# Kernel tuning notes

Measured on AMD Instinct MI355X. Metric: run time of the kernel, lower is better.

Reference implementation:

```python
import jax, jax.numpy as jnp
from jax import lax
import numpy as np

C = 256; NH = 8; NP = 4; FFN = 512; B = 2; H = 128; W = 128
HD = C // NH


def _ln(x, g, b):
    m = jnp.mean(x, -1, keepdims=True)
    v = jnp.var(x, -1, keepdims=True)
    return (x - m) * lax.rsqrt(v + 1e-5) * g + b


def _deform_attn(q, kv, off_w, off_b, attw_w, attw_b, vp_w, vp_b, op_w, op_b):
    # q, kv: (B, N, C) with N = H*W
    Bn, N, Cc = q.shape
    val = (kv @ vp_w + vp_b).reshape(Bn, N, NH, HD)
    off = (q @ off_w + off_b).reshape(Bn, N, NH, NP, 2)
    attw = jax.nn.softmax((q @ attw_w + attw_b).reshape(Bn, N, NH, NP), axis=-1)
    # identity-grid reference points (normalized, pixel centers)
    ry = (jnp.arange(H, dtype=q.dtype) + 0.5) / H
    rx = (jnp.arange(W, dtype=q.dtype) + 0.5) / W
    gy, gx = jnp.meshgrid(ry, rx, indexing='ij')
    ref = jnp.stack([gx.ravel(), gy.ravel()], -1)  # (N, 2) as (x, y)
    norm = jnp.array([W, H], dtype=q.dtype)
    loc = ref[None, :, None, None, :] + off / norm  # (B,N,NH,NP,2) in [0,1]
    # grid_sample align_corners=False, zeros padding
    x = loc[..., 0] * W - 0.5
    y = loc[..., 1] * H - 0.5
    x0 = jnp.floor(x); y0 = jnp.floor(y)
    lx = x - x0; ly = y - y0
    x0i = x0.astype(jnp.int32); y0i = y0.astype(jnp.int32)
    v_t = val.transpose(0, 2, 1, 3)  # (B, NH, N, HD)

    def gather(xi, yi, w):
        valid = (xi >= 0) & (xi < W) & (yi >= 0) & (yi < H)
        idx = jnp.clip(yi, 0, H - 1) * W + jnp.clip(xi, 0, W - 1)  # (B,N,NH,NP)
        idx_t = idx.transpose(0, 2, 1, 3).reshape(Bn, NH, N * NP)
        g = jnp.take_along_axis(v_t, idx_t[..., None], axis=2)
        g = g.reshape(Bn, NH, N, NP, HD)
        wm = (w * valid).transpose(0, 2, 1, 3)  # (B,NH,N,NP)
        return g * wm[..., None]

    samp = (gather(x0i, y0i, (1 - lx) * (1 - ly))
            + gather(x0i + 1, y0i, lx * (1 - ly))
            + gather(x0i, y0i + 1, (1 - lx) * ly)
            + gather(x0i + 1, y0i + 1, lx * ly))  # (B,NH,N,NP,HD)
    out = jnp.einsum('bhnpd,bnhp->bnhd', samp, attw).reshape(Bn, N, Cc)
    return out @ op_w + op_b


def _forward(cam_bev, sat_bev,
             c2s_off_w, c2s_off_b, c2s_attw_w, c2s_attw_b, c2s_vp_w, c2s_vp_b, c2s_op_w, c2s_op_b,
             s2c_off_w, s2c_off_b, s2c_attw_w, s2c_attw_b, s2c_vp_w, s2c_vp_b, s2c_op_w, s2c_op_b,
             ln1_g, ln1_b, ln2_g, ln2_b, lnf_g, lnf_b,
             ffn1_w, ffn1_b, ffn2_w, ffn2_b,
             g1_w, bn_g, bn_b, g2_w, g2_b):
    Bn, Cc, Hh, Ww = cam_bev.shape
    q_cam = cam_bev.reshape(Bn, Cc, Hh * Ww).transpose(0, 2, 1)
    q_sat = sat_bev.reshape(Bn, Cc, Hh * Ww).transpose(0, 2, 1)
    c2s = _deform_attn(q_cam, q_sat, c2s_off_w, c2s_off_b, c2s_attw_w, c2s_attw_b,
                       c2s_vp_w, c2s_vp_b, c2s_op_w, c2s_op_b)
    cam_att = _ln(q_cam + c2s, ln1_g, ln1_b)
    s2c = _deform_attn(q_sat, q_cam, s2c_off_w, s2c_off_b, s2c_attw_w, s2c_attw_b,
                       s2c_vp_w, s2c_vp_b, s2c_op_w, s2c_op_b)
    sat_att = _ln(q_sat + s2c, ln2_g, ln2_b)
    cam_map = cam_att.transpose(0, 2, 1).reshape(Bn, Cc, Hh, Ww)
    sat_map = sat_att.transpose(0, 2, 1).reshape(Bn, Cc, Hh, Ww)
    gi = jnp.concatenate([cam_map, sat_map], axis=1)
    h = lax.conv_general_dilated(gi, g1_w, (1, 1), 'SAME',
                                 dimension_numbers=('NCHW', 'OIHW', 'NCHW'))
    # BatchNorm2d in eval mode: running_mean=0, running_var=1
    h = jax.nn.relu(h * lax.rsqrt(jnp.float32(1.0 + 1e-5)) * bn_g[None, :, None, None]
                    + bn_b[None, :, None, None])
    g = jax.nn.sigmoid(jnp.einsum('bchw,oc->bohw', h, g2_w) + g2_b[None, :, None, None])
    fused = g * cam_map + (1 - g) * sat_map
    ff = fused.reshape(Bn, Cc, Hh * Ww).transpose(0, 2, 1)
    ff = ff + (jax.nn.relu(ff @ ffn1_w + ffn1_b) @ ffn2_w + ffn2_b)
    ff = _ln(ff, lnf_g, lnf_b)
    return ff.transpose(0, 2, 1).reshape(Bn, Cc, Hh, Ww) + cam_bev


def setup_inputs() -> dict:
    key = jax.random.key(0)
    ks = iter(jax.random.split(key, 40))

    def rn(shape, s=0.02):
        return jax.random.normal(next(ks), shape, jnp.float32) * s

    # directional offset-bias init (as in original init_weights)
    thetas = np.arange(NH) * (2.0 * np.pi / NH)
    grid = np.stack([np.cos(thetas), np.sin(thetas)], -1)
    grid = grid / np.abs(grid).max(-1, keepdims=True)
    grid = np.tile(grid[:, None, :], (1, NP, 1)) * np.arange(1, NP + 1)[None, :, None]
    off_bias = jnp.asarray(grid.reshape(-1), jnp.float32)

    def attn_params():
        return dict(off_w=rn((C, NH * NP * 2), 0.01), off_b=off_bias,
                    attw_w=rn((C, NH * NP), 0.02), attw_b=rn((NH * NP,), 0.02),
                    vp_w=rn((C, C), 0.05), vp_b=jnp.zeros((C,), jnp.float32),
                    op_w=rn((C, C), 0.05), op_b=jnp.zeros((C,), jnp.float32))

    p1 = attn_params(); p2 = attn_params()
    inp = {
        'cam_bev': jax.random.normal(next(ks), (B, C, H, W), jnp.float32),
        'sat_bev': jax.random.normal(next(ks), (B, C, H, W), jnp.float32),
    }
    for pre, p in (('c2s_', p1), ('s2c_', p2)):
        for k, v in p.items():
            inp[pre + k] = v
    inp.update(
        ln1_g=jnp.ones((C,), jnp.float32), ln1_b=jnp.zeros((C,), jnp.float32),
        ln2_g=jnp.ones((C,), jnp.float32), ln2_b=jnp.zeros((C,), jnp.float32),
        lnf_g=jnp.ones((C,), jnp.float32), lnf_b=jnp.zeros((C,), jnp.float32),
        ffn1_w=rn((C, FFN), 0.05), ffn1_b=jnp.zeros((FFN,), jnp.float32),
        ffn2_w=rn((FFN, C), 0.05), ffn2_b=jnp.zeros((C,), jnp.float32),
        g1_w=rn((C // 2, 2 * C, 3, 3), 0.02),
        bn_g=jnp.ones((C // 2,), jnp.float32), bn_b=jnp.zeros((C // 2,), jnp.float32),
        g2_w=rn((C, C // 2), 0.02), g2_b=jnp.zeros((C,), jnp.float32),
    )
    return inp


def reference(cam_bev, sat_bev,
              c2s_off_w, c2s_off_b, c2s_attw_w, c2s_attw_b, c2s_vp_w, c2s_vp_b, c2s_op_w, c2s_op_b,
              s2c_off_w, s2c_off_b, s2c_attw_w, s2c_attw_b, s2c_vp_w, s2c_vp_b, s2c_op_w, s2c_op_b,
              ln1_g, ln1_b, ln2_g, ln2_b, lnf_g, lnf_b,
              ffn1_w, ffn1_b, ffn2_w, ffn2_b,
              g1_w, bn_g, bn_b, g2_w, g2_b):
    return _forward(cam_bev, sat_bev,
                    c2s_off_w, c2s_off_b, c2s_attw_w, c2s_attw_b, c2s_vp_w, c2s_vp_b, c2s_op_w, c2s_op_b,
                    s2c_off_w, s2c_off_b, s2c_attw_w, s2c_attw_b, s2c_vp_w, s2c_vp_b, s2c_op_w, s2c_op_b,
                    ln1_g, ln1_b, ln2_g, ln2_b, lnf_g, lnf_b,
                    ffn1_w, ffn1_b, ffn2_w, ffn2_b,
                    g1_w, bn_g, bn_b, g2_w, g2_b)
```

## Files before the change

### kernel.cpp

```cpp
#include <hip/hip_runtime.h>
#include <hip/hip_bf16.h>
#include <cstddef>

#define BBn  2
#define CCn  256
#define HHn  128
#define WWn  128
#define NNn  (HHn*WWn)
#define MTOT (BBn*NNn)
#define PADW 130

typedef unsigned short u16;
typedef __attribute__((ext_vector_type(8))) short bf8v;
typedef __attribute__((ext_vector_type(8))) unsigned short u16x8;
typedef __attribute__((ext_vector_type(4))) float f4v;

typedef __attribute__((address_space(1))) const void gvoid_t;
typedef __attribute__((address_space(3))) void svoid_t;
#define ASYNC16(g, l) __builtin_amdgcn_global_load_lds((gvoid_t*)(g), (svoid_t*)(l), 16, 0, 0)

__device__ __forceinline__ u16 f2bf(float f) {
    __hip_bfloat16 h = __float2bfloat16(f);
    return *reinterpret_cast<u16*>(&h);
}
__device__ __forceinline__ float bf2f(u16 h) {
    return __uint_as_float(((unsigned)h) << 16);
}

struct ZOff {
    long a, w, bia, f1, f2, b1, r, p;
    int ch;
};

template<int BM, int BN, int WC, int EPI, int KK>
__global__ __launch_bounds__(256)
void mgemm(const u16* __restrict__ A, const u16* __restrict__ Wt,
           const float* __restrict__ bias, int ldw, int Nc,
           float* __restrict__ outf, float* __restrict__ outf2,
           u16* __restrict__ outb, const u16* __restrict__ img,
           const void* __restrict__ resid,
           const float* __restrict__ p0, const float* __restrict__ p1,
           int choff, ZOff zo)
{
    constexpr int WR = 4 / WC;
    constexpr int MROWS = BM / WR;
    constexpr int MI = MROWS / 16;
    constexpr int AT = BM / 64;
    constexpr int BT = BN / 64;

    __shared__ __align__(16) u16 As[BM * 32];
    __shared__ __align__(16) u16 Bs[BN * 32];
    __shared__ float red[4][64][2];

    const int z = blockIdx.z;
    if (z) {
        A += (long)z * zo.a; Wt += (long)z * zo.w;
        if (bias)  bias  += (long)z * zo.bia;
        if (outf)  outf  += (long)z * zo.f1;
        if (outf2) outf2 += (long)z * zo.f2;
        if (outb)  outb  += (long)z * zo.b1;
        if (p0)    p0    += (long)z * zo.p;
        if (p1)    p1    += (long)z * zo.p;
        choff += z * zo.ch;
    }

    const int tid  = threadIdx.x;
    const int lane = tid & 63;
    const int w    = tid >> 6;
    const int wr   = w / WC, wc = w % WC;
    const int by = blockIdx.y;
    const int m0 = by * BM;
    const int n0 = blockIdx.x * BN;
    const int lr = lane & 15, lq = lane >> 4;
    const int kb = lq * 8;

    const u16* gA[AT];
    #pragma unroll
    for (int t = 0; t < AT; ++t) {
        int c = t * 256 + tid; int row = c >> 2; int part = c & 3;
        gA[t] = A + (size_t)(m0 + row) * KK + part * 8;
    }
    const u16* gB[BT];
    #pragma unroll
    for (int t = 0; t < BT; ++t) {
        int c = t * 256 + tid; int row = c >> 2; int part = c & 3;
        gB[t] = Wt + (size_t)(n0 + row) * ldw + part * 8;
    }

    f4v acc[MI][4];
    if constexpr (EPI == 7 || EPI == 9) {
        const u16* r16 = (const u16*)resid + (EPI == 7 ? (long)z * zo.r : 0);
        #pragma unroll
        for (int j = 0; j < 4; ++j) {
            int n = wc * 64 + j * 16 + lr;
            float bj = bias[n];
            #pragma unroll
            for (int i = 0; i < MI; ++i)
                #pragma unroll
                for (int r = 0; r < 4; ++r) {
                    int m = m0 + i * 16 + lq * 4 + r;
                    acc[i][j][r] = bf2f(r16[(size_t)m * 256 + n]) + bj;
                }
        }
    } else {
        #pragma unroll
        for (int i = 0; i < MI; ++i)
            #pragma unroll
            for (int j = 0; j < 4; ++j)
                acc[i][j] = (f4v){0.f, 0.f, 0.f, 0.f};
    }

    for (int k0 = 0; k0 < KK; k0 += 32) {
        #pragma unroll
        for (int t = 0; t < AT; ++t)
            ASYNC16(gA[t] + k0, (u16*)As + (t * 256 + tid) * 8);
        #pragma unroll
        for (int t = 0; t < BT; ++t)
            ASYNC16(gB[t] + k0, (u16*)Bs + (t * 256 + tid) * 8);
        __syncthreads();

        bf8v af[MI], bv[4];
        #pragma unroll
        for (int i = 0; i < MI; ++i)
            af[i] = *(const bf8v*)&As[(wr * MROWS + i * 16 + lr) * 32 + kb];
        #pragma unroll
        for (int j = 0; j < 4; ++j)
            bv[j] = *(const bf8v*)&Bs[(wc * 64 + j * 16 + lr) * 32 + kb];
        #pragma unroll
        for (int i = 0; i < MI; ++i)
            #pragma unroll
            for (int j = 0; j < 4; ++j)
                acc[i][j] = __builtin_amdgcn_mfma_f32_16x16x32_bf16(af[i], bv[j], acc[i][j], 0, 0, 0);
        __syncthreads();
    }

    if constexpr (EPI == 7 || EPI == 9) {
        float g4[4], b4[4];
        #pragma unroll
        for (int j = 0; j < 4; ++j) {
            int n = wc * 64 + j * 16 + lr;
            g4[j] = p0[n]; b4[j] = p1[n];
        }
        #pragma unroll
        for (int i = 0; i < MI; ++i)
            #pragma unroll
            for (int r = 0; r < 4; ++r) {
                float p = 0.f, p2 = 0.f;
                #pragma unroll
                for (int j = 0; j < 4; ++j) { float v = acc[i][j][r]; p += v; p2 += v * v; }
                p += __shfl_xor(p, 1, 16);  p2 += __shfl_xor(p2, 1, 16);
                p += __shfl_xor(p, 2, 16);  p2 += __shfl_xor(p2, 2, 16);
                p += __shfl_xor(p, 4, 16);  p2 += __shfl_xor(p2, 4, 16);
                p += __shfl_xor(p, 8, 16);  p2 += __shfl_xor(p2, 8, 16);
                if (lr == 0) {
                    int row = i * 16 + lq * 4 + r;
                    red[w][row][0] = p; red[w][row][1] = p2;
                }
            }
        __syncthreads();
        #pragma unroll
        for (int i = 0; i < MI; ++i) {
            float mean4[4], rstd4[4];
            #pragma unroll
            for (int r = 0; r < 4; ++r) {
                int row = i * 16 + lq * 4 + r;
                float s  = red[0][row][0] + red[1][row][0] + red[2][row][0] + red[3][row][0];
                float s2 = red[0][row][1] + red[1][row][1] + red[2][row][1] + red[3][row][1];
                float mean = s * (1.f / 256.f);
                float var  = s2 * (1.f / 256.f) - mean * mean;
                mean4[r] = mean;
                rstd4[r] = rsqrtf(var + 1e-5f);
            }
            if constexpr (EPI == 7) {
                #pragma unroll
                for (int r = 0; r < 4; ++r) {
                    int m = m0 + i * 16 + lq * 4 + r;
                    int b = m >> 14, sp = m & (NNn - 1);
                    size_t pb = (((size_t)b * PADW + (sp >> 7) + 1) * PADW + (sp & 127) + 1) * 512 + choff;
                    #pragma unroll
                    for (int j = 0; j < 4; ++j) {
                        int n = wc * 64 + j * 16 + lr;
                        outb[pb + n] = f2bf((acc[i][j][r] - mean4[r]) * rstd4[r] * g4[j] + b4[j]);
                    }
                }
            } else {
                int mb = m0 + i * 16 + lq * 4;
                int b = mb >> 14, sp = mb & (NNn - 1);
                #pragma unroll
                for (int j = 0; j < 4; ++j) {
                    int n = wc * 64 + j * 16 + lr;
                    size_t oi = ((size_t)b * 256 + n) * NNn + sp;
                    float4 cv = *(const float4*)&outf2[oi];
                    float4 o;
                    o.x = (acc[i][j][0] - mean4[0]) * rstd4[0] * g4[j] + b4[j] + cv.x;
                    o.y = (acc[i][j][1] - mean4[1]) * rstd4[1] * g4[j] + b4[j] + cv.y;
                    o.z = (acc[i][j][2] - mean4[2]) * rstd4[2] * g4[j] + b4[j] + cv.z;
                    o.w = (acc[i][j][3] - mean4[3]) * rstd4[3] * g4[j] + b4[j] + cv.w;
                    *(float4*)&outf[oi] = o;
                }
            }
        }
        return;
    }

    float bj[4]; int ncol[4];
    #pragma unroll
    for (int j = 0; j < 4; ++j) {
        int n = n0 + wc * 64 + j * 16 + lr;
        ncol[j] = n;
        if constexpr (EPI == 0 || EPI == 4 || EPI == 5) bj[j] = bias[n];
    }
    #pragma unroll
    for (int i = 0; i < MI; ++i) {
        #pragma unroll
        for (int r = 0; r < 4; ++r) {
            int m = m0 + wr * MROWS + i * 16 + lq * 4 + r;
            size_t pb = 0;
            if constexpr (EPI == 4) {
                int b = m >> 14, sp = m & (NNn - 1);
                pb = (((size_t)b * PADW + (sp >> 7) + 1) * PADW + (sp & 127) + 1) * 512;
            }
            #pragma unroll
            for (int j = 0; j < 4; ++j) {
                int n = ncol[j];
                float v = acc[i][j][r];
                size_t oi = (size_t)m * Nc + n;
                if constexpr (EPI == 0) {
                    outb[oi] = f2bf(v + bj[j]);
                } else if constexpr (EPI == 2) {
                    if (n < 64)      outf [(size_t)m * 64 + n]        = v + p0[n];
                    else if (n < 96) outf2[(size_t)m * 32 + (n - 64)] = v + p1[n - 64];
                } else if constexpr (EPI == 4) {
                    float vv = v + bj[j];
                    float g = 1.f / (1.f + __expf(-vv));
                    float f = g * bf2f(img[pb + n]) + (1.f - g) * bf2f(img[pb + 256 + n]);
                    outb[oi] = f2bf(f);
                } else if constexpr (EPI == 5) {
                    outb[oi] = f2bf(fmaxf(v + bj[j], 0.f));
                }
            }
        }
    }
}

template<int TAPS>
__global__ __launch_bounds__(256)
void conv_k(const u16* __restrict__ img, const u16* __restrict__ Wt,
            float* __restrict__ outp)
{
    __shared__ __align__(16) u16 As[128 * 64];
    __shared__ __align__(16) u16 Bs[128 * 64];

    const int z = blockIdx.z;
    outp += (size_t)z * MTOT * 128;
    const int tid = threadIdx.x;
    const int lane = tid & 63;
    const int w = tid >> 6;
    const int wr = w >> 1, wc = w & 1;
    int by = blockIdx.y;
    by = ((by & 7) << 5) | (by >> 3);
    const int m0 = by * 128;
    const int lr = lane & 15, lq = lane >> 4;

    long cbA[4]; int pgA[4]; const u16* wB[4]; int ldsOff[4];
    #pragma unroll
    for (int t = 0; t < 4; ++t) {
        int c = t * 256 + tid;
        int row = c >> 3, part = c & 7;
        int pg = part ^ (row & 7);
        ldsOff[t] = c * 8;
        int m = m0 + row; int b = m >> 14; int sp = m & (NNn - 1);
        cbA[t] = ((long)b * PADW + (sp >> 7)) * PADW + (sp & 127);
        pgA[t] = pg;
        wB[t] = Wt + (size_t)row * 4608 + pg * 8;
    }

    f4v acc[4][4];
    #pragma unroll
    for (int i = 0; i < 4; ++i)
        #pragma unroll
        for (int j = 0; j < 4; ++j)
            acc[i][j] = (f4v){0.f, 0.f, 0.f, 0.f};

    const int tap0 = z * TAPS;
    #pragma unroll
    for (int tt = 0; tt < TAPS; ++tt) {
        int tap = tap0 + tt;
        int dy = tap / 3, dx = tap - dy * 3;
        const u16* bpA[4]; const u16* bpB[4];
        #pragma unroll
        for (int t = 0; t < 4; ++t) {
            bpA[t] = img + (size_t)(cbA[t] + dy * PADW + dx) * 512 + pgA[t] * 8;
            bpB[t] = wB[t] + tap * 512;
        }
        #pragma unroll 2
        for (int ci = 0; ci < 512; ci += 64) {
            #pragma unroll
            for (int t = 0; t < 4; ++t)
                ASYNC16(bpA[t] + ci, (u16*)As + ldsOff[t]);
            #pragma unroll
            for (int t = 0; t < 4; ++t)
                ASYNC16(bpB[t] + ci, (u16*)Bs + ldsOff[t]);
            __syncthreads();
            #pragma unroll
            for (int kk = 0; kk < 2; ++kk) {
                bf8v af[4], bv[4];
                #pragma unroll
                for (int i = 0; i < 4; ++i) {
                    int row = wr * 64 + i * 16 + lr;
                    af[i] = *(const bf8v*)&As[(row * 8 + ((kk * 4 + lq) ^ (row & 7))) * 8];
                }
                #pragma unroll
                for (int j = 0; j < 4; ++j) {
                    int row = wc * 64 + j * 16 + lr;
                    bv[j] = *(const bf8v*)&Bs[(row * 8 + ((kk * 4 + lq) ^ (row & 7))) * 8];
                }
                #pragma unroll
                for (int i = 0; i < 4; ++i)
                    #pragma unroll
                    for (int j = 0; j < 4; ++j)
                        acc[i][j] = __builtin_amdgcn_mfma_f32_16x16x32_bf16(af[i], bv[j], acc[i][j], 0, 0, 0);
            }
            __syncthreads();
        }
    }

    #pragma unroll
    for (int i = 0; i < 4; ++i)
        #pragma unroll
        for (int r = 0; r < 4; ++r) {
            int m = m0 + wr * 64 + i * 16 + lq * 4 + r;
            #pragma unroll
            for (int j = 0; j < 4; ++j) {
                int n = wc * 64 + j * 16 + lr;
                outp[(size_t)m * 128 + n] = acc[i][j][r];
            }
        }
}

__global__ __launch_bounds__(256)
void combine_k(const float* __restrict__ part, const float* __restrict__ bng,
               const float* __restrict__ bnb, u16* __restrict__ hb)
{
    const float bnscale = rsqrtf(1.0f + 1e-5f);
    int i = (blockIdx.x * 256 + threadIdx.x) * 4;
    int n = i & 127;
    float4 a = *(const float4*)&part[i];
    float4 b = *(const float4*)&part[(size_t)MTOT * 128 + i];
    float4 c = *(const float4*)&part[(size_t)MTOT * 256 + i];
    ushort4 o;
    o.x = f2bf(fmaxf((a.x + b.x + c.x) * bnscale * bng[n + 0] + bnb[n + 0], 0.f));
    o.y = f2bf(fmaxf((a.y + b.y + c.y) * bnscale * bng[n + 1] + bnb[n + 1], 0.f));
    o.z = f2bf(fmaxf((a.z + b.z + c.z) * bnscale * bng[n + 2] + bnb[n + 2], 0.f));
    o.w = f2bf(fmaxf((a.w + b.w + c.w) * bnscale * bng[n + 3] + bnb[n + 3], 0.f));
    *(ushort4*)&hb[i] = o;
}

__global__ __launch_bounds__(256)
void tcvt_k(const float* __restrict__ cam, const float* __restrict__ sat,
            u16* __restrict__ qcam, u16* __restrict__ qsat)
{
    __shared__ float t[64][65];
    int z = blockIdx.z;
    const float* src = (z < 2) ? cam : sat;
    u16* dst = (z < 2) ? qcam : qsat;
    int b = z & 1;
    int c0 = blockIdx.x * 64, sp0 = blockIdx.y * 64;
    #pragma unroll
    for (int it = 0; it < 16; ++it) {
        int idx = it * 256 + threadIdx.x;
        int cl = idx >> 6, sl = idx & 63;
        t[cl][sl] = src[((size_t)(b * CCn + c0 + cl)) * NNn + sp0 + sl];
    }
    __syncthreads();
    #pragma unroll
    for (int it = 0; it < 16; ++it) {
        int idx = it * 256 + threadIdx.x;
        int sl = idx >> 6, cl = idx & 63;
        dst[((size_t)(b * NNn + sp0 + sl)) * CCn + c0 + cl] = f2bf(t[cl][sl]);
    }
}

__global__ __launch_bounds__(256)
void sample_k(const u16* __restrict__ val, const float* __restrict__ off,
              const float* __restrict__ lg, u16* __restrict__ outp)
{
    __shared__ uint2 desc[32][17];

    int z = blockIdx.z;
    val  += (size_t)z * MTOT * CCn;
    off  += (size_t)z * MTOT * 64;
    lg   += (size_t)z * MTOT * 32;
    outp += (size_t)z * MTOT * CCn;

    const int tid = threadIdx.x;
    const int rh0 = blockIdx.x * 32;

    if (tid < 32) {
        int rhg = rh0 + tid;
        int h = rhg & 7, rn = rhg >> 3;
        int n = rn & (NNn - 1), b = rn >> 14;
        int yp = n >> 7, xp = n & 127;

        const float* ofp = off + (size_t)rn * 64 + h * 8;
        const float* lgp = lg  + (size_t)rn * 32 + h * 4;
        float4 of0 = *(const float4*)ofp;
        float4 of1 = *(const float4*)(ofp + 4);
        float4 lgv = *(const float4*)lgp;
        float ofx[4] = { of0.x, of0.z, of1.x, of1.z };
        float ofy[4] = { of0.y, of0.w, of1.y, of1.w };

        float mx = fmaxf(fmaxf(lgv.x, lgv.y), fmaxf(lgv.z, lgv.w));
        float e0 = __expf(lgv.x - mx), e1 = __expf(lgv.y - mx);
        float e2 = __expf(lgv.z - mx), e3 = __expf(lgv.w - mx);
        float inv = 1.f / (e0 + e1 + e2 + e3);
        float aw[4] = { e0 * inv, e1 * inv, e2 * inv, e3 * inv };

        unsigned hb = (unsigned)(b * NNn) * 256u + h * 32;
        #pragma unroll
        for (int p = 0; p < 4; ++p) {
            float xs = (float)xp + ofx[p];
            float ys = (float)yp + ofy[p];
            float x0f = floorf(xs), y0f = floorf(ys);
            float lx = xs - x0f, ly = ys - y0f;
            int x0 = (int)x0f, y0 = (int)y0f;
            #pragma unroll
            for (int c = 0; c < 4; ++c) {
                int xi = x0 + (c & 1), yi = y0 + (c >> 1);
                bool valid = (xi >= 0) & (xi < WWn) & (yi >= 0) & (yi < HHn);
                float wgt = valid
                    ? aw[p] * ((c & 1) ? lx : 1.f - lx) * ((c >> 1) ? ly : 1.f - ly)
                    : 0.f;
                int xc = min(max(xi, 0), WWn - 1);
                int yc = min(max(yi, 0), HHn - 1);
                unsigned addr = hb + (unsigned)(yc * WWn + xc) * 256u;
                desc[tid][p * 4 + c] = make_uint2(addr, __float_as_uint(wgt));
            }
        }
    }
    __syncthreads();

    const int rh = tid >> 3;
    const int q  = tid & 7;
    const int rhg = rh0 + rh;
    const int h = rhg & 7, rn = rhg >> 3;

    float a0 = 0.f, a1 = 0.f, a2 = 0.f, a3 = 0.f;
    #pragma unroll
    for (int k = 0; k < 16; ++k) {
        uint2 d = desc[rh][k];
        float wgt = __uint_as_float(d.y);
        ushort4 v = *(const ushort4*)(val + d.x + q * 4);
        a0 += wgt * bf2f(v.x);
        a1 += wgt * bf2f(v.y);
        a2 += wgt * bf2f(v.z);
        a3 += wgt * bf2f(v.w);
    }
    ushort4 o;
    o.x = f2bf(a0); o.y = f2bf(a1); o.z = f2bf(a2); o.w = f2bf(a3);
    *(ushort4*)(outp + (size_t)rn * CCn + h * 32 + q * 4) = o;
}

__global__ __launch_bounds__(256)
void repack_all(const float* __restrict__ vp1, const float* __restrict__ op1,
                const float* __restrict__ vp2, const float* __restrict__ op2,
                const float* __restrict__ f1w, const float* __restrict__ f2w,
                const float* __restrict__ of1, const float* __restrict__ aw1,
                const float* __restrict__ of2, const float* __restrict__ aw2,
                const float* __restrict__ g1,  const float* __restrict__ g2,
                const float* __restrict__ vpb1, const float* __restrict__ vpb2,
                const float* __restrict__ opb1, const float* __restrict__ opb2,
                const float* __restrict__ ofb1, const float* __restrict__ awb1,
                const float* __restrict__ ofb2, const float* __restrict__ awb2,
                const float* __restrict__ l1g, const float* __restrict__ l1b,
                const float* __restrict__ l2g, const float* __restrict__ l2b,
                u16* __restrict__ wb, float* __restrict__ bb)
{
    int i = blockIdx.x * 256 + threadIdx.x;
    if (i >= 1212416 + 2240) return;
    if (i >= 1212416) {
        int j = i - 1212416;
        float v;
        if      (j < 256)  v = vpb1[j];
        else if (j < 512)  v = vpb2[j - 256];
        else if (j < 768)  v = opb1[j - 512];
        else if (j < 1024) v = opb2[j - 768];
        else if (j < 1088) v = ofb1[j - 1024];
        else if (j < 1120) v = awb1[j - 1088];
        else if (j < 1184) v = ofb2[j - 1120];
        else if (j < 1216) v = awb2[j - 1184];
        else if (j < 1472) v = l1g[j - 1216];
        else if (j < 1728) v = l1b[j - 1472];
        else if (j < 1984) v = l2g[j - 1728];
        else               v = l2b[j - 1984];
        bb[j] = v;
        return;
    }
    float v;
    if (i < 262144) {
        const float* src[4] = { vp1, vp2, op1, op2 };
        int q = i >> 16, j = i & 65535;
        int n = j >> 8, k = j & 255;
        v = src[q][(size_t)k * 256 + n];
    } else if (i < 393216) {
        int j = i - 262144; int n = j >> 8, k = j & 255;
        v = f1w[(size_t)k * 512 + n];
    } else if (i < 524288) {
        int j = i - 393216; int n = j >> 9, k = j & 511;
        v = f2w[(size_t)k * 256 + n];
    } else if (i < 589824) {
        int jj = i - 524288; int hh = jj >> 15; int j = jj & 32767;
        int n = j >> 8, k = j & 255;
        const float* ofw = hh ? of2 : of1;
        const float* aww = hh ? aw2 : aw1;
        if (n < 64)      v = ofw[(size_t)k * 64 + n];
        else if (n < 96) v = aww[(size_t)k * 32 + (n - 64)];
        else             v = 0.f;
    } else if (i < 1179648) {
        int j = i - 589824; int co = j / 4608, k = j - co * 4608;
        int tap = k >> 9, ci = k & 511;
        v = g1[((size_t)co * 512 + ci) * 9 + tap];
    } else {
        int j = i - 1179648; int n = j >> 7, k = j & 127;
        v = g2[(size_t)n * 128 + k];
    }
    wb[i] = f2bf(v);
}

extern "C" void kernel_launch(void* const* d_in, const int* in_sizes, int n_in,
                              void* d_out, int out_size, void* d_ws, size_t ws_size,
                              hipStream_t stream)
{
    const float* cam_bev   = (const float*)d_in[0];
    const float* sat_bev   = (const float*)d_in[1];
    const float* c2s_off_w  = (const float*)d_in[2];
    const float* c2s_off_b  = (const float*)d_in[3];
    const float* c2s_attw_w = (const float*)d_in[4];
    const float* c2s_attw_b = (const float*)d_in[5];
    const float* c2s_vp_w   = (const float*)d_in[6];
    const float* c2s_vp_b   = (const float*)d_in[7];
    const float* c2s_op_w   = (const float*)d_in[8];
    const float* c2s_op_b   = (const float*)d_in[9];
    const float* s2c_off_w  = (const float*)d_in[10];
    const float* s2c_off_b  = (const float*)d_in[11];
    const float* s2c_attw_w = (const float*)d_in[12];
    const float* s2c_attw_b = (const float*)d_in[13];
    const float* s2c_vp_w   = (const float*)d_in[14];
    const float* s2c_vp_b   = (const float*)d_in[15];
    const float* s2c_op_w   = (const float*)d_in[16];
    const float* s2c_op_b   = (const float*)d_in[17];
    const float* ln1_g = (const float*)d_in[18];
    const float* ln1_b = (const float*)d_in[19];
    const float* ln2_g = (const float*)d_in[20];
    const float* ln2_b = (const float*)d_in[21];
    const float* lnf_g = (const float*)d_in[22];
    const float* lnf_b = (const float*)d_in[23];
    const float* ffn1_w = (const float*)d_in[24];
    const float* ffn1_b = (const float*)d_in[25];
    const float* ffn2_w = (const float*)d_in[26];
    const float* ffn2_b = (const float*)d_in[27];
    const float* g1_w  = (const float*)d_in[28];
    const float* bn_g  = (const float*)d_in[29];
    const float* bn_b  = (const float*)d_in[30];
    const float* g2_w  = (const float*)d_in[31];
    const float* g2_b  = (const float*)d_in[32];

    char* base = (char*)d_ws;
    size_t off = 0;
    auto alloc = [&](size_t bytes) -> void* {
        void* p = base + off;
        off += (bytes + 255) & ~(size_t)255;
        return p;
    };

    u16*   qcam   = (u16*)  alloc((size_t)MTOT * CCn * 2 * 2);
    u16*   qsat   = qcam + (size_t)MTOT * CCn;
    u16*   valb   = (u16*)  alloc((size_t)MTOT * CCn * 2 * 2);
    u16*   sampb  = (u16*)  alloc((size_t)MTOT * CCn * 2 * 2);
    float* offb   = (float*)alloc((size_t)MTOT * 64 * 4 * 2);
    float* attwb  = (float*)alloc((size_t)MTOT * 32 * 4 * 2);
    size_t padBytes = (size_t)BBn * PADW * PADW * 512 * 2;
    u16*   pad    = (u16*)  alloc(padBytes);
    u16*   hbuf   = (u16*)  alloc((size_t)MTOT * 128 * 2);
    u16*   wbase  = (u16*)  alloc((size_t)1212416 * 2);
    float* biasbf = (float*)alloc((size_t)2240 * 4);
    u16* wvp = wbase;
    u16* wop = wbase + 131072;
    u16* wf1 = wbase + 262144;
    u16* wf2 = wbase + 393216;
    u16* woa = wbase + 524288;
    u16* wcv = wbase + 589824;
    u16* wg2 = wbase + 1179648;
    u16*   fused_bf = valb;
    float* convpart = (float*)sampb;
    u16*   midb     = qcam;

    dim3 blk(256);
    ZOff zz{0, 0, 0, 0, 0, 0, 0, 0, 0};

    hipMemsetAsync(pad, 0, padBytes, stream);
    tcvt_k<<<dim3(4, 256, 4), blk, 0, stream>>>(cam_bev, sat_bev, qcam, qsat);
    repack_all<<<4746, blk, 0, stream>>>(c2s_vp_w, c2s_op_w, s2c_vp_w, s2c_op_w,
                                         ffn1_w, ffn2_w, c2s_off_w, c2s_attw_w,
                                         s2c_off_w, s2c_attw_w, g1_w, g2_w,
                                         c2s_vp_b, s2c_vp_b, c2s_op_b, s2c_op_b,
                                         c2s_off_b, c2s_attw_b, s2c_off_b, s2c_attw_b,
                                         ln1_g, ln1_b, ln2_g, ln2_b,
                                         wbase, biasbf);

    {
        ZOff zo{ -(long)MTOT * CCn, 65536, 256, 0, 0, (long)MTOT * CCn, 0, 0, 0 };
        mgemm<128, 128, 2, 0, 256><<<dim3(2, 256, 2), blk, 0, stream>>>(
            qsat, wvp, biasbf, 256, 256,
            nullptr, nullptr, valb, nullptr, nullptr, nullptr, nullptr, 0, zo);
    }
    {
        ZOff zo{ (long)MTOT * CCn, 32768, 0, (long)MTOT * 64, (long)MTOT * 32, 0, 0, 96, 0 };
        mgemm<128, 128, 2, 2, 256><<<dim3(1, 256, 2), blk, 0, stream>>>(
            qcam, woa, nullptr, 256, 128,
            offb, attwb, nullptr, nullptr, nullptr, biasbf + 1024, biasbf + 1088, 0, zo);
    }
    sample_k<<<dim3(8192, 1, 2), blk, 0, stream>>>(valb, offb, attwb, sampb);
    {
        ZOff zo{ (long)MTOT * CCn, 65536, 256, 0, 0, 0, (long)MTOT * CCn, 512, 256 };
        mgemm<64, 256, 4, 7, 256><<<dim3(1, 512, 2), blk, 0, stream>>>(
            sampb, wop, biasbf + 512, 256, 256,
            nullptr, nullptr, pad, nullptr, qcam, biasbf + 1216, biasbf + 1472, 0, zo);
    }
    conv_k<3><<<dim3(1, 256, 3), blk, 0, stream>>>(pad, wcv, convpart);
    combine_k<<<4096, blk, 0, stream>>>(convpart, bn_g, bn_b, hbuf);

    mgemm<128, 128, 2, 4, 128><<<dim3(2, 256, 1), blk, 0, stream>>>(
        hbuf, wg2, g2_b, 128, 256,
        nullptr, nullptr, fused_bf, pad, nullptr, nullptr, nullptr, 0, zz);

    mgemm<128, 128, 2, 5, 256><<<dim3(4, 256, 1), blk, 0, stream>>>(
        fused_bf, wf1, ffn1_b, 256, 512,
        nullptr, nullptr, midb, nullptr, nullptr, nullptr, nullptr, 0, zz);
    mgemm<64, 256, 4, 9, 512><<<dim3(1, 512, 1), blk, 0, stream>>>(
        midb, wf2, ffn2_b, 512, 256,
        (float*)d_out, (float*)cam_bev, nullptr, nullptr, fused_bf, lnf_g, lnf_b, 0, zz);
}
```

Baseline: 306.0 us.

## Double-buffer LDS tiles in GEMM and conv kernels with swizzled layout

Both the generic MFMA GEMM and the implicit-GEMM conv kernel now use two LDS buffers, issuing the async global-to-LDS load for the next K step before computing the current one. This overlaps memory latency with MFMA work and removes one barrier per step. The conv K tile shrinks from 64 to 32 so the doubled buffers fit in the same LDS footprint. An XOR swizzle on the 32-wide rows is added to avoid LDS bank conflicts. Trade-offs: the conv kernel runs twice as many steps with smaller tiles, its fully unrolled loop grows code size, and the async loads rely on a single barrier per step for ordering.

```diff
diff --git a/kernel.cpp b/kernel.cpp
--- a/kernel.cpp
+++ b/kernel.cpp
@@ -47,9 +47,10 @@
     constexpr int MI = MROWS / 16;
     constexpr int AT = BM / 64;
     constexpr int BT = BN / 64;
-
-    __shared__ __align__(16) u16 As[BM * 32];
-    __shared__ __align__(16) u16 Bs[BN * 32];
+    constexpr int NSTEPS = KK / 32;
+
+    __shared__ __align__(16) u16 As[2 * BM * 32];
+    __shared__ __align__(16) u16 Bs[2 * BN * 32];
     __shared__ float red[4][64][2];
 
     const int z = blockIdx.z;
@@ -72,19 +73,22 @@
     const int m0 = by * BM;
     const int n0 = blockIdx.x * BN;
     const int lr = lane & 15, lq = lane >> 4;
-    const int kb = lq * 8;
-
-    const u16* gA[AT];
+
+    const u16* gA[AT]; int loA[AT];
     #pragma unroll
     for (int t = 0; t < AT; ++t) {
         int c = t * 256 + tid; int row = c >> 2; int part = c & 3;
-        gA[t] = A + (size_t)(m0 + row) * KK + part * 8;
-    }
-    const u16* gB[BT];
+        int pg = part ^ ((row >> 1) & 3);
+        gA[t] = A + (size_t)(m0 + row) * KK + pg * 8;
+        loA[t] = c * 8;
+    }
+    const u16* gB[BT]; int loB[BT];
     #pragma unroll
     for (int t = 0; t < BT; ++t) {
         int c = t * 256 + tid; int row = c >> 2; int part = c & 3;
-        gB[t] = Wt + (size_t)(n0 + row) * ldw + part * 8;
+        int pg = part ^ ((row >> 1) & 3);
+        gB[t] = Wt + (size_t)(n0 + row) * ldw + pg * 8;
+        loB[t] = c * 8;
     }
 
     f4v acc[MI][4];
@@ -110,29 +114,44 @@
                 acc[i][j] = (f4v){0.f, 0.f, 0.f, 0.f};
     }
 
-    for (int k0 = 0; k0 < KK; k0 += 32) {
+    auto stageG = [&](int s, int buf) {
+        int k0 = s * 32;
         #pragma unroll
         for (int t = 0; t < AT; ++t)
-            ASYNC16(gA[t] + k0, (u16*)As + (t * 256 + tid) * 8);
+            ASYNC16(gA[t] + k0, (u16*)As + buf * (BM * 32) + loA[t]);
         #pragma unroll
         for (int t = 0; t < BT; ++t)
-            ASYNC16(gB[t] + k0, (u16*)Bs + (t * 256 + tid) * 8);
-        __syncthreads();
-
+            ASYNC16(gB[t] + k0, (u16*)Bs + buf * (BN * 32) + loB[t]);
+    };
+    auto computeStep = [&](int s) {
+        const u16* Ab = As + (s & 1) * (BM * 32);
+        const u16* Bb = Bs + (s & 1) * (BN * 32);
         bf8v af[MI], bv[4];
         #pragma unroll
-        for (int i = 0; i < MI; ++i)
-            af[i] = *(const bf8v*)&As[(wr * MROWS + i * 16 + lr) * 32 + kb];
-        #pragma unroll
-        for (int j = 0; j < 4; ++j)
-            bv[j] = *(const bf8v*)&Bs[(wc * 64 + j * 16 + lr) * 32 + kb];
+        for (int i = 0; i < MI; ++i) {
+            int row = wr * MROWS + i * 16 + lr;
+            af[i] = *(const bf8v*)&Ab[row * 32 + ((lq ^ ((row >> 1) & 3)) << 3)];
+        }
+        #pragma unroll
+        for (int j = 0; j < 4; ++j) {
+            int row = wc * 64 + j * 16 + lr;
+            bv[j] = *(const bf8v*)&Bb[row * 32 + ((lq ^ ((row >> 1) & 3)) << 3)];
+        }
         #pragma unroll
         for (int i = 0; i < MI; ++i)
             #pragma unroll
             for (int j = 0; j < 4; ++j)
                 acc[i][j] = __builtin_amdgcn_mfma_f32_16x16x32_bf16(af[i], bv[j], acc[i][j], 0, 0, 0);
+    };
+
+    stageG(0, 0);
+    __syncthreads();
+    for (int s = 0; s < NSTEPS - 1; ++s) {
+        stageG(s + 1, (s + 1) & 1);
+        computeStep(s);
         __syncthreads();
     }
+    computeStep(NSTEPS - 1);
 
     if constexpr (EPI == 7 || EPI == 9) {
         float g4[4], b4[4];
@@ -248,8 +267,9 @@
 void conv_k(const u16* __restrict__ img, const u16* __restrict__ Wt,
             float* __restrict__ outp)
 {
-    __shared__ __align__(16) u16 As[128 * 64];
-    __shared__ __align__(16) u16 Bs[128 * 64];
+    constexpr int NS = TAPS * 16;
+    __shared__ __align__(16) u16 As[2 * 128 * 32];
+    __shared__ __align__(16) u16 Bs[2 * 128 * 32];
 
     const int z = blockIdx.z;
     outp += (size_t)z * MTOT * 128;
@@ -262,17 +282,26 @@
     const int m0 = by * 128;
     const int lr = lane & 15, lq = lane >> 4;
 
-    long cbA[4]; int pgA[4]; const u16* wB[4]; int ldsOff[4];
-    #pragma unroll
-    for (int t = 0; t < 4; ++t) {
+    const u16* abase[2]; const u16* bbase[2]; int ldsOff[2];
+    #pragma unroll
+    for (int t = 0; t < 2; ++t) {
         int c = t * 256 + tid;
-        int row = c >> 3, part = c & 7;
-        int pg = part ^ (row & 7);
+        int row = c >> 2, part = c & 3;
+        int pg = part ^ ((row >> 1) & 3);
         ldsOff[t] = c * 8;
         int m = m0 + row; int b = m >> 14; int sp = m & (NNn - 1);
-        cbA[t] = ((long)b * PADW + (sp >> 7)) * PADW + (sp & 127);
-        pgA[t] = pg;
-        wB[t] = Wt + (size_t)row * 4608 + pg * 8;
+        long cb = ((long)b * PADW + (sp >> 7)) * PADW + (sp & 127);
+        abase[t] = img + cb * 512 + pg * 8;
+        bbase[t] = Wt + (size_t)row * 4608 + pg * 8;
+    }
+
+    long adel[TAPS]; int bdel[TAPS];
+    #pragma unroll
+    for (int tt = 0; tt < TAPS; ++tt) {
+        int tap = z * TAPS + tt;
+        int dy = tap / 3, dx = tap - dy * 3;
+        adel[tt] = (long)(dy * PADW + dx) * 512;
+        bdel[tt] = tap * 512;
     }
 
     f4v acc[4][4];
@@ -282,48 +311,45 @@
         for (int j = 0; j < 4; ++j)
             acc[i][j] = (f4v){0.f, 0.f, 0.f, 0.f};
 
-    const int tap0 = z * TAPS;
-    #pragma unroll
-    for (int tt = 0; tt < TAPS; ++tt) {
-        int tap = tap0 + tt;
-        int dy = tap / 3, dx = tap - dy * 3;
-        const u16* bpA[4]; const u16* bpB[4];
-        #pragma unroll
-        for (int t = 0; t < 4; ++t) {
-            bpA[t] = img + (size_t)(cbA[t] + dy * PADW + dx) * 512 + pgA[t] * 8;
-            bpB[t] = wB[t] + tap * 512;
-        }
-        #pragma unroll 2
-        for (int ci = 0; ci < 512; ci += 64) {
-            #pragma unroll
-            for (int t = 0; t < 4; ++t)
-                ASYNC16(bpA[t] + ci, (u16*)As + ldsOff[t]);
-            #pragma unroll
-            for (int t = 0; t < 4; ++t)
-                ASYNC16(bpB[t] + ci, (u16*)Bs + ldsOff[t]);
-            __syncthreads();
-            #pragma unroll
-            for (int kk = 0; kk < 2; ++kk) {
-                bf8v af[4], bv[4];
-                #pragma unroll
-                for (int i = 0; i < 4; ++i) {
-                    int row = wr * 64 + i * 16 + lr;
-                    af[i] = *(const bf8v*)&As[(row * 8 + ((kk * 4 + lq) ^ (row & 7))) * 8];
-                }
-                #pragma unroll
-                for (int j = 0; j < 4; ++j) {
-                    int row = wc * 64 + j * 16 + lr;
-                    bv[j] = *(const bf8v*)&Bs[(row * 8 + ((kk * 4 + lq) ^ (row & 7))) * 8];
-                }
-                #pragma unroll
-                for (int i = 0; i < 4; ++i)
-                    #pragma unroll
-                    for (int j = 0; j < 4; ++j)
-                        acc[i][j] = __builtin_amdgcn_mfma_f32_16x16x32_bf16(af[i], bv[j], acc[i][j], 0, 0, 0);
-            }
-            __syncthreads();
-        }
-    }
+    auto stage = [&](int s, int buf) {
+        int tt = s >> 4;
+        int ci = (s & 15) * 32;
+        #pragma unroll
+        for (int t = 0; t < 2; ++t) {
+            ASYNC16(abase[t] + adel[tt] + ci, (u16*)As + buf * (128 * 32) + ldsOff[t]);
+            ASYNC16(bbase[t] + bdel[tt] + ci, (u16*)Bs + buf * (128 * 32) + ldsOff[t]);
+        }
+    };
+    auto computeStep = [&](int s) {
+        const u16* Ab = As + (s & 1) * (128 * 32);
+        const u16* Bb = Bs + (s & 1) * (128 * 32);
+        bf8v af[4], bv[4];
+        #pragma unroll
+        for (int i = 0; i < 4; ++i) {
+            int row = wr * 64 + i * 16 + lr;
+            af[i] = *(const bf8v*)&Ab[row * 32 + ((lq ^ ((row >> 1) & 3)) << 3)];
+        }
+        #pragma unroll
+        for (int j = 0; j < 4; ++j) {
+            int row = wc * 64 + j * 16 + lr;
+            bv[j] = *(const bf8v*)&Bb[row * 32 + ((lq ^ ((row >> 1) & 3)) << 3)];
+        }
+        #pragma unroll
+        for (int i = 0; i < 4; ++i)
+            #pragma unroll
+            for (int j = 0; j < 4; ++j)
+                acc[i][j] = __builtin_amdgcn_mfma_f32_16x16x32_bf16(af[i], bv[j], acc[i][j], 0, 0, 0);
+    };
+
+    stage(0, 0);
+    __syncthreads();
+    #pragma unroll
+    for (int s = 0; s < NS - 1; ++s) {
+        stage(s + 1, (s + 1) & 1);
+        computeStep(s);
+        __syncthreads();
+    }
+    computeStep(NS - 1);
 
     #pragma unroll
     for (int i = 0; i < 4; ++i)
```

Result: faster. 298.7 us (-2.4%).
